# Performance work log

Hardware: AMD Instinct MI355X
Metric: run time of the kernel (lower is better)

## Reference

```python
import jax, jax.numpy as jnp
import numpy as np

# dims: B graphs, NE entity nodes, NR relation nodes, N total nodes, D=hsz, H heads, P prop steps
B, NE, NR, D, H, P = 4, 1536, 512, 128, 4, 2
N = NE + NR
DH = D // H
RV = 500  # relation vocab
EPS = 1e-5


def setup_inputs() -> dict:
    key = jax.random.key(0)
    ks = jax.random.split(key, 20)
    s = 0.02
    inp = {
        "vents": jax.random.normal(ks[0], (B, NE, D), dtype=jnp.float32),
        "rels": jax.random.randint(ks[1], (B, NR), 0, RV),
        "adj": jax.random.randint(ks[2], (B, N, N), 0, 2, dtype=jnp.int32),
        "entlens": jnp.full((B,), NE, dtype=jnp.int32),
        "renc_w": jax.random.normal(ks[3], (RV, D), dtype=jnp.float32) * s,
        # per-prop-step attention params (torch Linear stored as [in, out])
        "Wq": jax.random.normal(ks[4], (P, D, D)) * s,
        "bq": jnp.zeros((P, D)),
        "Wk": jax.random.normal(ks[5], (P, D, D)) * s,
        "bk": jnp.zeros((P, D)),
        "Wv": jax.random.normal(ks[6], (P, D, D)) * s,
        "bv": jnp.zeros((P, D)),
        "Wo": jax.random.normal(ks[7], (P, D, D)) * s,
        "bo": jnp.zeros((P, D)),
        # Block FFN hsz -> 4*hsz -> hsz
        "l1_w": jax.random.normal(ks[8], (P, D, 4 * D)) * s,
        "l1_b": jnp.zeros((P, 4 * D)),
        "l2_w": jax.random.normal(ks[9], (P, 4 * D, D)) * s,
        "l2_b": jnp.zeros((P, D)),
        # ln_1 is used for BOTH norms in Block (faithful to original bug)
        "ln_g": jnp.ones((P, D)),
        "ln_b": jnp.zeros((P, D)),
        # PReLU per-channel slope, torch default 0.25
        "prelu_a": jnp.full((P, 4 * D), 0.25, dtype=jnp.float32),
    }
    return inp


def _ln(x, g, b):
    m = x.mean(-1, keepdims=True)
    v = ((x - m) ** 2).mean(-1, keepdims=True)
    return (x - m) / jnp.sqrt(v + EPS) * g + b


def reference(vents, rels, adj, entlens, renc_w,
              Wq, bq, Wk, bk, Wv, bv, Wo, bo,
              l1_w, l1_b, l2_w, l2_b, ln_g, ln_b, prelu_a):
    # vgraph_i = cat(vents[i][:entlens[i]], renc(rels[i])) -> all graphs same size, batched
    vgraph = jnp.concatenate([vents, renc_w[rels]], axis=1)  # [B, N, D]
    mask = (adj == 0)  # [B, N, N] True = masked out
    scale = 1.0 / np.sqrt(DH).astype(np.float32)
    for p in range(P):
        q_in = vgraph
        kv_in = jax.lax.stop_gradient(vgraph)  # dense path: ngraph is detached
        Q = (q_in @ Wq[p] + bq[p]).reshape(B, N, H, DH)
        K = (kv_in @ Wk[p] + bk[p]).reshape(B, N, H, DH)
        V = (kv_in @ Wv[p] + bv[p]).reshape(B, N, H, DH)
        scores = jnp.einsum('bihd,bjhd->bhij', Q, K) * scale  # [B, H, N, N]
        scores = jnp.where(mask[:, None, :, :], -1e9, scores)
        A = jax.nn.softmax(scores, axis=-1)
        O = jnp.einsum('bhij,bjhd->bihd', A, V).reshape(B, N, D) @ Wo[p] + bo[p]
        # Block feed-forward (dropout = identity in eval)
        t = _ln(O, ln_g[p], ln_b[p])
        h1 = t @ l1_w[p] + l1_b[p]
        h1 = jnp.where(h1 >= 0, h1, prelu_a[p] * h1)  # PReLU
        q2 = h1 @ l2_w[p] + l2_b[p]
        vgraph = _ln(q2 + t, ln_g[p], ln_b[p])
    glob = vgraph[jnp.arange(B), entlens]  # vgraph[entlens[i]] per graph -> [B, D]
    gents = vgraph  # all graphs same length, no padding needed -> [B, N, D]
    emask = jnp.ones((B, N), dtype=bool)  # arange(N) <= N is all True
    return glob, gents, emask
```

## Files before the change

kernel.cpp:

```cpp
#include <hip/hip_runtime.h>
#include <hip/hip_bf16.h>

typedef __bf16 bf16;
typedef __bf16 bf16x4 __attribute__((ext_vector_type(4)));
typedef __bf16 bf16x8 __attribute__((ext_vector_type(8)));
typedef float f32x4 __attribute__((ext_vector_type(4)));
typedef float f32x16 __attribute__((ext_vector_type(16)));

#define B_ 4
#define NE_ 1536
#define NR_ 512
#define N_ 2048
#define D_ 128
#define H_ 4
#define DH_ 32
#define P_ 2
#define M_ (B_*N_)
#define NW_ (N_/32)
#define SK_ 4
#define KCH_ (N_/SK_)
#define NIT_ (KCH_/64)

__device__ __forceinline__ f32x4 mfma16(bf16x8 a, bf16x8 b, f32x4 c) {
    return __builtin_amdgcn_mfma_f32_16x16x32_bf16(a, b, c, 0, 0, 0);
}
__device__ __forceinline__ f32x16 mfma32(bf16x8 a, bf16x8 b, f32x16 c) {
    return __builtin_amdgcn_mfma_f32_32x32x16_bf16(a, b, c, 0, 0, 0);
}
__device__ __forceinline__ unsigned cvtpk(float lo, float hi) {
    unsigned r;
    asm("v_cvt_pk_bf16_f32 %0, %1, %2" : "=v"(r) : "v"(lo), "v"(hi));
    return r;
}
__device__ __forceinline__ void swap32(unsigned& a, unsigned& b) {
    asm("v_permlane32_swap_b32 %0, %1" : "+v"(a), "+v"(b));
}
__device__ __forceinline__ void gload16(const void* g, void* l) {
    __builtin_amdgcn_global_load_lds(
        (const __attribute__((address_space(1))) void*)g,
        (__attribute__((address_space(3))) void*)l, 16, 0, 0);
}

__device__ __forceinline__ size_t fragidx(int c, int i, int K) {
    int nb = c >> 4, kc = i >> 5;
    int l = ((i >> 3) & 3) * 16 + (c & 15);
    return ((size_t)(nb * (K >> 5) + kc) * 64 + l) * 8 + (i & 7);
}

#define VGN_ (B_*N_*D_)
#define MKN_ (B_*N_*NW_)
#define PPER_ (3*16384 + 16384 + 65536 + 65536 + 384)
#define PRN_ (P_*PPER_)
__global__ void k_prep(const float* __restrict__ vents, const int* __restrict__ rels,
                       const float* __restrict__ renc, const int* __restrict__ adj,
                       const float* __restrict__ Wq, const float* __restrict__ Wk,
                       const float* __restrict__ Wv, const float* __restrict__ Wo,
                       const float* __restrict__ l1w, const float* __restrict__ l2w,
                       const float* __restrict__ bq, const float* __restrict__ bk,
                       const float* __restrict__ bv,
                       bf16* __restrict__ vb, unsigned int* __restrict__ mw,
                       bf16* __restrict__ wqkvT, float* __restrict__ bqkv,
                       bf16* __restrict__ woT, bf16* __restrict__ l1T,
                       bf16* __restrict__ l2T) {
    const float SC = 0.25503330560513437f;
    int idx = blockIdx.x * 256 + threadIdx.x;
    if (idx < VGN_) {
        int d = idx & (D_ - 1);
        int n = (idx >> 7) & (N_ - 1);
        int b = idx >> 18;
        float v;
        if (n < NE_) v = vents[((size_t)(b * NE_ + n)) * D_ + d];
        else         v = renc[(size_t)rels[b * NR_ + (n - NE_)] * D_ + d];
        vb[idx] = (bf16)v;
        return;
    }
    idx -= VGN_;
    if (idx < MKN_) {
        const int4* a = (const int4*)(adj + (size_t)idx * 32);
        unsigned int w = 0;
#pragma unroll
        for (int q = 0; q < 8; ++q) {
            int4 t = a[q];
            w |= (t.x != 0 ? 1u : 0u) << (q * 4 + 0);
            w |= (t.y != 0 ? 1u : 0u) << (q * 4 + 1);
            w |= (t.z != 0 ? 1u : 0u) << (q * 4 + 2);
            w |= (t.w != 0 ? 1u : 0u) << (q * 4 + 3);
        }
        mw[idx] = w;
        return;
    }
    idx -= MKN_;
    if (idx >= PRN_) return;
    int p = idx / PPER_;
    int r = idx % PPER_;
    if (r < 3 * 16384) {
        int which = r / 16384, e = r % 16384;
        int o = e >> 7, i = e & 127;
        const float* W = which == 0 ? Wq : (which == 1 ? Wk : Wv);
        float v = W[(size_t)(p * 128 + i) * 128 + o];
        if (which == 0) v *= SC;
        wqkvT[(size_t)p * 384 * 128 + fragidx(which * 128 + o, i, 128)] = (bf16)v;
    } else if ((r -= 3 * 16384) < 16384) {
        int o = r >> 7, i = r & 127;
        woT[(size_t)p * 16384 + fragidx(o, i, 128)] = (bf16)Wo[(size_t)(p * 128 + i) * 128 + o];
    } else if ((r -= 16384) < 65536) {
        int o = r >> 7, i = r & 127;
        l1T[(size_t)p * 65536 + fragidx(o, i, 128)] = (bf16)l1w[(size_t)(p * 128 + i) * 512 + o];
    } else if ((r -= 65536) < 65536) {
        int o = r >> 9, i = r & 511;
        l2T[(size_t)p * 65536 + fragidx(o, i, 512)] = (bf16)l2w[(size_t)(p * 512 + i) * 128 + o];
    } else {
        r -= 65536;
        float v = r < 128 ? bq[p * 128 + r] * SC
                          : (r < 256 ? bk[p * 128 + r - 128] : bv[p * 128 + r - 256]);
        bqkv[p * 384 + r] = v;
    }
}

__global__ __launch_bounds__(256) void k_qkv(
        const bf16* __restrict__ X, const bf16* __restrict__ WT,
        const float* __restrict__ bias,
        bf16* __restrict__ Qout, bf16* __restrict__ Kout,
        bf16* __restrict__ VTout) {
    int lane = threadIdx.x & 63, wid = threadIdx.x >> 6;
    int wr = wid >> 1, wc = wid & 1;
    int m0 = blockIdx.x * 64 + wr * 32;
    int n0 = blockIdx.y * 64 + wc * 32;
    int lr = lane & 15, lg = lane >> 4;
    f32x4 acc[2][2];
#pragma unroll
    for (int mi = 0; mi < 2; ++mi)
#pragma unroll
        for (int ni = 0; ni < 2; ++ni)
            acc[mi][ni] = f32x4{0.f, 0.f, 0.f, 0.f};

    for (int k0 = 0; k0 < 128; k0 += 32) {
        int kc = k0 >> 5;
        bf16x8 a[2], bb[2];
#pragma unroll
        for (int mi = 0; mi < 2; ++mi)
            a[mi] = *(const bf16x8*)(X + (size_t)(m0 + mi * 16 + lr) * 128 + k0 + lg * 8);
#pragma unroll
        for (int ni = 0; ni < 2; ++ni) {
            int nb = (n0 >> 4) + ni;
            bb[ni] = *(const bf16x8*)(WT + ((size_t)(nb * 4 + kc) * 64 + lane) * 8);
        }
#pragma unroll
        for (int mi = 0; mi < 2; ++mi)
#pragma unroll
            for (int ni = 0; ni < 2; ++ni)
                acc[mi][ni] = mfma16(a[mi], bb[ni], acc[mi][ni]);
    }
#pragma unroll
    for (int mi = 0; mi < 2; ++mi) {
#pragma unroll
        for (int ni = 0; ni < 2; ++ni) {
            int col = n0 + ni * 16 + lr;
            float bs = bias[col];
            int rowb = m0 + mi * 16 + lg * 4;
            if (col < 128) {
#pragma unroll
                for (int r = 0; r < 4; ++r)
                    Qout[(size_t)(rowb + r) * D_ + col] = (bf16)(acc[mi][ni][r] + bs);
            } else if (col < 256) {
#pragma unroll
                for (int r = 0; r < 4; ++r)
                    Kout[(size_t)(rowb + r) * D_ + (col - 128)] = (bf16)(acc[mi][ni][r] + bs);
            } else {
                int d = col - 256, h = d >> 5, dh = d & 31;
                int b = rowb >> 11, nn = rowb & (N_ - 1);
                bf16x4 pk;
#pragma unroll
                for (int r = 0; r < 4; ++r) pk[r] = (bf16)(acc[mi][ni][r] + bs);
                *(bf16x4*)(VTout + ((size_t)(b * H_ + h) * DH_ + dh) * N_ + nn) = pk;
            }
        }
    }
}

__global__ __launch_bounds__(256) void k_attn(
    const bf16* __restrict__ Q, const bf16* __restrict__ Kt,
    const bf16* __restrict__ VT, const unsigned int* __restrict__ mw,
    bf16* __restrict__ partO, float* __restrict__ partML) {
    __shared__ __align__(16) char kbuf[3][4096];
    __shared__ __align__(16) char vbuf[3][4096];
    __shared__ __align__(16) unsigned mbuf[128][16];
    int wid = threadIdx.x >> 6;
    int lane = threadIdx.x & 63;
    int ql = lane & 31, hf = lane >> 5;
    int qx = blockIdx.x;
    int bh = blockIdx.y;
    int kc = blockIdx.z;
    int b = bh >> 2, h = bh & 3;
    int qg = qx * 128 + wid * 32 + ql;
    const size_t bnD = (size_t)b * N_ * D_;

    const bf16* qp = Q + bnD + (size_t)qg * D_ + h * 32 + hf * 8;
    bf16x8 qf0 = *(const bf16x8*)(qp);
    bf16x8 qf1 = *(const bf16x8*)(qp + 16);

#pragma unroll
    for (int j = 0; j < 2; ++j) {
        int u = threadIdx.x + 256 * j;
        int row = u >> 2, sub = u & 3;
        uint4 mv = *(const uint4*)(mw + ((size_t)b * N_ + qx * 128 + row) * NW_
                                      + kc * (KCH_ / 32) + sub * 4);
        *(uint4*)(&mbuf[row][sub * 4]) = mv;
    }
    asm volatile("s_waitcnt lgkmcnt(0)" ::: "memory");

    const char* kg = (const char*)(Kt + bnD + (size_t)(kc * KCH_) * D_) + h * 64;
    const char* vg = (const char*)(VT + (size_t)(bh * DH_) * N_ + kc * KCH_);

    f32x16 of;
#pragma unroll
    for (int i = 0; i < 16; ++i) of[i] = 0.f;
    const f32x16 zero16 = of;
    float lsum = 0.f;
    int mrow = wid * 32 + ql;

#define STAGE(bufi, it) do {                                                   \
        int k0s = (it) * 64;                                                   \
        gload16(kg + (size_t)(k0s + lane) * 256 + wid * 16,                    \
                kbuf[bufi] + wid * 1024);                                      \
        gload16(vg + ((size_t)(lane & 31) * N_ + k0s) * 2 +                    \
                    (2 * wid + (lane >> 5)) * 16,                              \
                vbuf[bufi] + wid * 1024);                                      \
    } while (0)

    STAGE(0, 0);
    STAGE(1, 1);
    __builtin_amdgcn_s_barrier();

    unsigned long long mcur = *(const unsigned long long*)(&mbuf[mrow][0]);

#pragma unroll 1
    for (int it = 0; it < NIT_; ++it) {
        int cur = it % 3;
        const char* kb_ = kbuf[cur];
        const char* vb_ = vbuf[cur];
        if (it < NIT_ - 1) asm volatile("s_waitcnt vmcnt(2)" ::: "memory");
        else               asm volatile("s_waitcnt vmcnt(0)" ::: "memory");
        __builtin_amdgcn_s_barrier();
        __builtin_amdgcn_sched_barrier(0);
        if (it + 2 < NIT_) STAGE((it + 2) % 3, it + 2);

        unsigned long long mnext = (it + 1 < NIT_)
            ? *(const unsigned long long*)(&mbuf[mrow][(it + 1) * 2]) : 0ull;
        unsigned mw0 = (unsigned)mcur, mw1 = (unsigned)(mcur >> 32);

#pragma unroll
        for (int kb = 0; kb < 2; ++kb) {
            bf16x8 kf0 = *(const bf16x8*)(kb_ + hf * 1024 + (kb * 32 + ql) * 16);
            bf16x8 kf1 = *(const bf16x8*)(kb_ + 2048 + hf * 1024 + (kb * 32 + ql) * 16);
            f32x16 s = mfma32(kf0, qf0, zero16);
            s = mfma32(kf1, qf1, s);

            unsigned wsh = (kb ? mw1 : mw0) >> (hf * 4);
            float p[16];
#pragma unroll
            for (int r = 0; r < 16; ++r) {
                int bitp = (r & 3) + 8 * (r >> 2);
                float e = __builtin_amdgcn_exp2f(s[r]);
                p[r] = ((wsh >> bitp) & 1u) ? e : 0.f;
            }
            float a0 = (p[0] + p[1]) + (p[2] + p[3]);
            float a1 = (p[4] + p[5]) + (p[6] + p[7]);
            float a2 = (p[8] + p[9]) + (p[10] + p[11]);
            float a3 = (p[12] + p[13]) + (p[14] + p[15]);
            lsum += (a0 + a1) + (a2 + a3);

            unsigned lo0 = cvtpk(p[0], p[1]),   hi0 = cvtpk(p[2], p[3]);
            unsigned lo1 = cvtpk(p[4], p[5]),   hi1 = cvtpk(p[6], p[7]);
            unsigned lo2 = cvtpk(p[8], p[9]),   hi2 = cvtpk(p[10], p[11]);
            unsigned lo3 = cvtpk(p[12], p[13]), hi3 = cvtpk(p[14], p[15]);
            swap32(lo0, lo1); swap32(hi0, hi1);
            swap32(lo2, lo3); swap32(hi2, hi3);
            union { unsigned u[4]; bf16x8 v; } f0, f1;
            f0.u[0] = lo0; f0.u[1] = hi0; f0.u[2] = lo1; f0.u[3] = hi1;
            f1.u[0] = lo2; f1.u[1] = hi2; f1.u[2] = lo3; f1.u[3] = hi3;

            bf16x8 va = *(const bf16x8*)(vb_ + ((kb * 2 + 0) * 2 + hf) * 512 + ql * 16);
            bf16x8 vb2 = *(const bf16x8*)(vb_ + ((kb * 2 + 1) * 2 + hf) * 512 + ql * 16);
            __builtin_amdgcn_s_setprio(1);
            of = mfma32(va, f0.v, of);
            of = mfma32(vb2, f1.v, of);
            __builtin_amdgcn_s_setprio(0);
        }
        mcur = mnext;
    }
#undef STAGE

    lsum += __shfl_xor(lsum, 32, 64);
    size_t pb = ((size_t)(kc * 16 + bh) * N_ + qg) * 32;
#pragma unroll
    for (int g = 0; g < 4; ++g) {
        union { unsigned u[2]; bf16x4 v; } pk;
        pk.u[0] = cvtpk(of[4 * g + 0], of[4 * g + 1]);
        pk.u[1] = cvtpk(of[4 * g + 2], of[4 * g + 3]);
        *(bf16x4*)(partO + pb + 8 * g + 4 * hf) = pk.v;
    }
    if (lane < 32)
        partML[(size_t)(kc * 16 + bh) * N_ + qg] = lsum;
}

template <bool LAST>
__global__ __launch_bounds__(512) void k_ffn(
        const bf16* __restrict__ partO, const float* __restrict__ partML,
        const bf16* __restrict__ woT, const float* __restrict__ bo,
        const bf16* __restrict__ l1T, const float* __restrict__ l1b,
        const float* __restrict__ pra,
        const bf16* __restrict__ l2T, const float* __restrict__ l2b,
        const float* __restrict__ lng, const float* __restrict__ lnb,
        const bf16* __restrict__ wqkvT2, const float* __restrict__ bqkv2,
        const int* __restrict__ entl, float* __restrict__ gout,
        bf16* __restrict__ Qout, bf16* __restrict__ Kout,
        bf16* __restrict__ VTout) {
    __shared__ __align__(16) char Obuf[16 * 256];
    __shared__ __align__(16) char Tbuf[16 * 256];
    __shared__ __align__(16) char Hbuf[16 * 1024];
    __shared__ float lst[8][16][2];
    int t = threadIdx.x;
    int lane = t & 63, wid = t >> 6;
    int lr = lane & 15, lg = lane >> 4;
    int m0 = blockIdx.x * 16;

    {
        int i = t >> 5, u = t & 31;
        int r = m0 + i, b = r >> 11, q = r & (N_ - 1);
        int h = u >> 3, dh4 = u & 7;
        int bh = b * 4 + h;
        float L = 0.f;
        f32x4 o = {0.f, 0.f, 0.f, 0.f};
#pragma unroll
        for (int kc = 0; kc < SK_; ++kc) {
            size_t base = (size_t)(kc * 16 + bh) * N_ + q;
            L += partML[base];
            bf16x4 pv = *(const bf16x4*)(partO + base * 32 + dh4 * 4);
#pragma unroll
            for (int j = 0; j < 4; ++j) o[j] += (float)pv[j];
        }
        float rL = 1.f / L;
        bf16x4 pk;
#pragma unroll
        for (int j = 0; j < 4; ++j) pk[j] = (bf16)(o[j] * rL);
        *(bf16x4*)(Obuf + i * 256 + ((u * 8) ^ ((i & 7) << 4))) = pk;
    }
    __syncthreads();

    float tvx[4];
    {
        f32x4 acc = {0.f, 0.f, 0.f, 0.f};
#pragma unroll
        for (int k0 = 0; k0 < 128; k0 += 32) {
            bf16x8 a = *(const bf16x8*)(Obuf + lr * 256 + (((k0 + lg * 8) * 2) ^ ((lr & 7) << 4)));
            bf16x8 bb = *(const bf16x8*)(woT + ((size_t)(wid * 4 + (k0 >> 5)) * 64 + lane) * 8);
            acc = mfma16(a, bb, acc);
        }
        int col = wid * 16 + lr;
        float bs = bo[col];
#pragma unroll
        for (int r2 = 0; r2 < 4; ++r2) tvx[r2] = acc[r2] + bs;
#pragma unroll
        for (int r2 = 0; r2 < 4; ++r2) {
            float sv = tvx[r2], qv = tvx[r2] * tvx[r2];
#pragma unroll
            for (int msk = 1; msk < 16; msk <<= 1) {
                sv += __shfl_xor(sv, msk, 64);
                qv += __shfl_xor(qv, msk, 64);
            }
            if (lr == 0) { lst[wid][lg * 4 + r2][0] = sv; lst[wid][lg * 4 + r2][1] = qv; }
        }
        __syncthreads();
#pragma unroll
        for (int r2 = 0; r2 < 4; ++r2) {
            int row = lg * 4 + r2;
            float S = 0.f, Q2 = 0.f;
#pragma unroll
            for (int w2 = 0; w2 < 8; ++w2) { S += lst[w2][row][0]; Q2 += lst[w2][row][1]; }
            float mean = S * (1.f / 128.f);
            float var = Q2 * (1.f / 128.f) - mean * mean;
            float rstd = rsqrtf(var + 1e-5f);
            float o = (tvx[r2] - mean) * rstd * lng[col] + lnb[col];
            tvx[r2] = o;
            *(bf16*)(Tbuf + row * 256 + ((col * 2) ^ ((row & 7) << 4))) = (bf16)o;
        }
    }
    __syncthreads();

    {
        f32x4 acc[4];
#pragma unroll
        for (int ni = 0; ni < 4; ++ni) acc[ni] = f32x4{0.f, 0.f, 0.f, 0.f};
#pragma unroll
        for (int k0 = 0; k0 < 128; k0 += 32) {
            bf16x8 a = *(const bf16x8*)(Tbuf + lr * 256 + (((k0 + lg * 8) * 2) ^ ((lr & 7) << 4)));
#pragma unroll
            for (int ni = 0; ni < 4; ++ni) {
                bf16x8 bb = *(const bf16x8*)(l1T + ((size_t)((wid * 4 + ni) * 4 + (k0 >> 5)) * 64 + lane) * 8);
                acc[ni] = mfma16(a, bb, acc[ni]);
            }
        }
#pragma unroll
        for (int ni = 0; ni < 4; ++ni) {
            int col = wid * 64 + ni * 16 + lr;
            float bs = l1b[col], sl = pra[col];
#pragma unroll
            for (int r2 = 0; r2 < 4; ++r2) {
                int row = lg * 4 + r2;
                float v = acc[ni][r2] + bs;
                v = v >= 0.f ? v : sl * v;
                *(bf16*)(Hbuf + row * 1024 + ((col * 2) ^ ((row & 7) << 4))) = (bf16)v;
            }
        }
    }
    __syncthreads();

    {
        f32x4 acc = {0.f, 0.f, 0.f, 0.f};
#pragma unroll
        for (int k0 = 0; k0 < 512; k0 += 32) {
            bf16x8 a = *(const bf16x8*)(Hbuf + lr * 1024 + (((k0 + lg * 8) * 2) ^ ((lr & 7) << 4)));
            bf16x8 bb = *(const bf16x8*)(l2T + ((size_t)(wid * 16 + (k0 >> 5)) * 64 + lane) * 8);
            acc = mfma16(a, bb, acc);
        }
        int col = wid * 16 + lr;
        float bs = l2b[col];
        float vx[4];
#pragma unroll
        for (int r2 = 0; r2 < 4; ++r2)
            vx[r2] = acc[r2] + bs + tvx[r2];
        __syncthreads();
#pragma unroll
        for (int r2 = 0; r2 < 4; ++r2) {
            float sv = vx[r2], qv = vx[r2] * vx[r2];
#pragma unroll
            for (int msk = 1; msk < 16; msk <<= 1) {
                sv += __shfl_xor(sv, msk, 64);
                qv += __shfl_xor(qv, msk, 64);
            }
            if (lr == 0) { lst[wid][lg * 4 + r2][0] = sv; lst[wid][lg * 4 + r2][1] = qv; }
        }
        __syncthreads();
#pragma unroll
        for (int r2 = 0; r2 < 4; ++r2) {
            int row = lg * 4 + r2;
            float S = 0.f, Q2 = 0.f;
#pragma unroll
            for (int w2 = 0; w2 < 8; ++w2) { S += lst[w2][row][0]; Q2 += lst[w2][row][1]; }
            float mean = S * (1.f / 128.f);
            float var = Q2 * (1.f / 128.f) - mean * mean;
            float rstd = rsqrtf(var + 1e-5f);
            float o = (vx[r2] - mean) * rstd * lng[col] + lnb[col];
            size_t rowg = (size_t)(m0 + row);
            if (LAST) {
                float* gents = gout + 512;
                gents[rowg * 128 + col] = o;
                int b = (int)(rowg >> 11);
                if ((int)(rowg & (N_ - 1)) == entl[b])
                    gout[b * 128 + col] = o;
            } else {
                *(bf16*)(Obuf + row * 256 + ((col * 2) ^ ((row & 7) << 4))) = (bf16)o;
            }
        }
        if (LAST && t < 16)
            gout[512 + (size_t)M_ * 128 + m0 + t] = 1.0f;
    }

    if (!LAST) {
        __syncthreads();
        f32x4 acc[3];
#pragma unroll
        for (int ni = 0; ni < 3; ++ni) acc[ni] = f32x4{0.f, 0.f, 0.f, 0.f};
#pragma unroll
        for (int k0 = 0; k0 < 128; k0 += 32) {
            bf16x8 a = *(const bf16x8*)(Obuf + lr * 256 + (((k0 + lg * 8) * 2) ^ ((lr & 7) << 4)));
#pragma unroll
            for (int ni = 0; ni < 3; ++ni) {
                bf16x8 bb = *(const bf16x8*)(wqkvT2 + ((size_t)((wid * 3 + ni) * 4 + (k0 >> 5)) * 64 + lane) * 8);
                acc[ni] = mfma16(a, bb, acc[ni]);
            }
        }
#pragma unroll
        for (int ni = 0; ni < 3; ++ni) {
            int col = wid * 48 + ni * 16 + lr;
            float bs = bqkv2[col];
            int rowb = m0 + lg * 4;
            if (col < 128) {
#pragma unroll
                for (int r = 0; r < 4; ++r)
                    Qout[(size_t)(rowb + r) * D_ + col] = (bf16)(acc[ni][r] + bs);
            } else if (col < 256) {
#pragma unroll
                for (int r = 0; r < 4; ++r)
                    Kout[(size_t)(rowb + r) * D_ + (col - 128)] = (bf16)(acc[ni][r] + bs);
            } else {
                int d = col - 256, h = d >> 5, dh = d & 31;
                int b = rowb >> 11, nn = rowb & (N_ - 1);
                bf16x4 pk;
#pragma unroll
                for (int r = 0; r < 4; ++r) pk[r] = (bf16)(acc[ni][r] + bs);
                *(bf16x4*)(VTout + ((size_t)(b * H_ + h) * DH_ + dh) * N_ + nn) = pk;
            }
        }
    }
}

extern "C" void kernel_launch(void* const* d_in, const int* in_sizes, int n_in,
                              void* d_out, int out_size, void* d_ws, size_t ws_size,
                              hipStream_t stream) {
    const float* vents = (const float*)d_in[0];
    const int*   rels  = (const int*)d_in[1];
    const int*   adj   = (const int*)d_in[2];
    const int*   entl  = (const int*)d_in[3];
    const float* renc  = (const float*)d_in[4];
    const float* Wq = (const float*)d_in[5];
    const float* bq = (const float*)d_in[6];
    const float* Wk = (const float*)d_in[7];
    const float* bk = (const float*)d_in[8];
    const float* Wv = (const float*)d_in[9];
    const float* bv = (const float*)d_in[10];
    const float* Wo = (const float*)d_in[11];
    const float* bo = (const float*)d_in[12];
    const float* l1w = (const float*)d_in[13];
    const float* l1b = (const float*)d_in[14];
    const float* l2w = (const float*)d_in[15];
    const float* l2b = (const float*)d_in[16];
    const float* lng = (const float*)d_in[17];
    const float* lnb = (const float*)d_in[18];
    const float* pra = (const float*)d_in[19];

    char* w = (char*)d_ws;
    auto alloc = [&](size_t bytes) { char* r = w; w += (bytes + 255) & ~(size_t)255; return r; };
    bf16*  vb    = (bf16*)alloc((size_t)M_ * D_ * 2);
    unsigned int* mw = (unsigned int*)alloc((size_t)B_ * N_ * NW_ * 4);
    bf16*  wqkvT = (bf16*)alloc((size_t)P_ * 384 * 128 * 2);
    float* bqkv  = (float*)alloc((size_t)P_ * 384 * 4);
    bf16*  woT   = (bf16*)alloc((size_t)P_ * 128 * 128 * 2);
    bf16*  l1T   = (bf16*)alloc((size_t)P_ * 512 * 128 * 2);
    bf16*  l2T   = (bf16*)alloc((size_t)P_ * 128 * 512 * 2);
    bf16*  Qb    = (bf16*)alloc((size_t)M_ * D_ * 2);
    bf16*  Kb    = (bf16*)alloc((size_t)M_ * D_ * 2);
    bf16*  VTb   = (bf16*)alloc((size_t)M_ * D_ * 2);
    bf16*  partO  = (bf16*)alloc((size_t)SK_ * 16 * N_ * 32 * 2);
    float* partML = (float*)alloc((size_t)SK_ * 16 * N_ * 4);
    float* gout  = (float*)d_out;

    const int PRTOT = VGN_ + MKN_ + PRN_;
    k_prep<<<(PRTOT + 255) / 256, 256, 0, stream>>>(
        vents, rels, renc, adj, Wq, Wk, Wv, Wo, l1w, l2w, bq, bk, bv,
        vb, mw, wqkvT, bqkv, woT, l1T, l2T);
    k_qkv<<<dim3(M_ / 64, 384 / 64), 256, 0, stream>>>(
        vb, wqkvT, bqkv, Qb, Kb, VTb);
    k_attn<<<dim3(16, 16, SK_), 256, 0, stream>>>(Qb, Kb, VTb, mw, partO, partML);
    k_ffn<false><<<M_ / 16, 512, 0, stream>>>(
        partO, partML, woT, bo, l1T, l1b, pra, l2T, l2b, lng, lnb,
        wqkvT + (size_t)384 * 128, bqkv + 384, entl, nullptr, Qb, Kb, VTb);
    k_attn<<<dim3(16, 16, SK_), 256, 0, stream>>>(Qb, Kb, VTb, mw, partO, partML);
    k_ffn<true><<<M_ / 16, 512, 0, stream>>>(
        partO, partML, woT + (size_t)16384, bo + 128,
        l1T + (size_t)65536, l1b + 512, pra + 512,
        l2T + (size_t)65536, l2b + 128, lng + 128, lnb + 128,
        wqkvT, bqkv, entl, gout, Qb, Kb, VTb);
}
```

Measured before the change: 108.3 us.

## Fuse first-step QKV projection into prep kernel and pad attention mask LDS

Removes the separate k_qkv launch and the bf16 vgraph staging buffer. The first propagation step's QKV GEMM now runs inside k_prep: it gathers fp32 rows straight from vents or the relation embedding table and converts weights on the fly, in the same launch as the mask packing and weight transposition. This saves one kernel launch and a full activation round trip through memory. In exchange, the weight loads are strided, uncoalesced scalar fp32 reads repeated by every block. Separately, the attention mask LDS rows are padded from 16 to 18 words, with stores split into 8-byte halves, to reduce bank conflicts.

```diff
diff --git a/kernel.cpp b/kernel.cpp
--- a/kernel.cpp
+++ b/kernel.cpp
@@ -47,34 +47,105 @@
     return ((size_t)(nb * (K >> 5) + kc) * 64 + l) * 8 + (i & 7);
 }
 
-#define VGN_ (B_*N_*D_)
+#define QKVB_ 768
 #define MKN_ (B_*N_*NW_)
 #define PPER_ (3*16384 + 16384 + 65536 + 65536 + 384)
 #define PRN_ (P_*PPER_)
-__global__ void k_prep(const float* __restrict__ vents, const int* __restrict__ rels,
-                       const float* __restrict__ renc, const int* __restrict__ adj,
-                       const float* __restrict__ Wq, const float* __restrict__ Wk,
-                       const float* __restrict__ Wv, const float* __restrict__ Wo,
-                       const float* __restrict__ l1w, const float* __restrict__ l2w,
-                       const float* __restrict__ bq, const float* __restrict__ bk,
-                       const float* __restrict__ bv,
-                       bf16* __restrict__ vb, unsigned int* __restrict__ mw,
-                       bf16* __restrict__ wqkvT, float* __restrict__ bqkv,
-                       bf16* __restrict__ woT, bf16* __restrict__ l1T,
-                       bf16* __restrict__ l2T) {
+__global__ __launch_bounds__(256) void k_prep(
+        const float* __restrict__ vents, const int* __restrict__ rels,
+        const float* __restrict__ renc, const int* __restrict__ adj,
+        const float* __restrict__ Wq, const float* __restrict__ Wk,
+        const float* __restrict__ Wv, const float* __restrict__ Wo,
+        const float* __restrict__ l1w, const float* __restrict__ l2w,
+        const float* __restrict__ bq, const float* __restrict__ bk,
+        const float* __restrict__ bv,
+        unsigned int* __restrict__ mw,
+        bf16* __restrict__ wqkvT, float* __restrict__ bqkv,
+        bf16* __restrict__ woT, bf16* __restrict__ l1T,
+        bf16* __restrict__ l2T,
+        bf16* __restrict__ Qout, bf16* __restrict__ Kout,
+        bf16* __restrict__ VTout) {
     const float SC = 0.25503330560513437f;
-    int idx = blockIdx.x * 256 + threadIdx.x;
-    if (idx < VGN_) {
-        int d = idx & (D_ - 1);
-        int n = (idx >> 7) & (N_ - 1);
-        int b = idx >> 18;
-        float v;
-        if (n < NE_) v = vents[((size_t)(b * NE_ + n)) * D_ + d];
-        else         v = renc[(size_t)rels[b * NR_ + (n - NE_)] * D_ + d];
-        vb[idx] = (bf16)v;
+    if (blockIdx.x < QKVB_) {
+        int qb = blockIdx.x;
+        int mt = qb / 6, nt = qb % 6;
+        int lane = threadIdx.x & 63, wid = threadIdx.x >> 6;
+        int wr = wid >> 1, wc = wid & 1;
+        int m0 = mt * 64 + wr * 32;
+        int n0 = nt * 64 + wc * 32;
+        int lr = lane & 15, lg = lane >> 4;
+        const float* srcA[2];
+#pragma unroll
+        for (int mi = 0; mi < 2; ++mi) {
+            int row = m0 + mi * 16 + lr;
+            int n = row & (N_ - 1), b = row >> 11;
+            srcA[mi] = (n < NE_) ? vents + ((size_t)(b * NE_ + n)) * D_
+                                 : renc + (size_t)rels[b * NR_ + (n - NE_)] * D_;
+        }
+        f32x4 acc[2][2];
+#pragma unroll
+        for (int mi = 0; mi < 2; ++mi)
+#pragma unroll
+            for (int ni = 0; ni < 2; ++ni)
+                acc[mi][ni] = f32x4{0.f, 0.f, 0.f, 0.f};
+        for (int k0 = 0; k0 < 128; k0 += 32) {
+            bf16x8 a[2], bb[2];
+#pragma unroll
+            for (int mi = 0; mi < 2; ++mi) {
+                float4 f0 = *(const float4*)(srcA[mi] + k0 + lg * 8);
+                float4 f1 = *(const float4*)(srcA[mi] + k0 + lg * 8 + 4);
+                bf16x8 v;
+                v[0] = (bf16)f0.x; v[1] = (bf16)f0.y; v[2] = (bf16)f0.z; v[3] = (bf16)f0.w;
+                v[4] = (bf16)f1.x; v[5] = (bf16)f1.y; v[6] = (bf16)f1.z; v[7] = (bf16)f1.w;
+                a[mi] = v;
+            }
+#pragma unroll
+            for (int ni = 0; ni < 2; ++ni) {
+                int col = n0 + ni * 16 + lr;
+                int which = col >> 7, c0 = col & 127;
+                const float* W = which == 0 ? Wq : (which == 1 ? Wk : Wv);
+                float sc = which == 0 ? SC : 1.f;
+                bf16x8 v;
+#pragma unroll
+                for (int e = 0; e < 8; ++e)
+                    v[e] = (bf16)(W[(size_t)(k0 + lg * 8 + e) * 128 + c0] * sc);
+                bb[ni] = v;
+            }
+#pragma unroll
+            for (int mi = 0; mi < 2; ++mi)
+#pragma unroll
+                for (int ni = 0; ni < 2; ++ni)
+                    acc[mi][ni] = mfma16(a[mi], bb[ni], acc[mi][ni]);
+        }
+#pragma unroll
+        for (int mi = 0; mi < 2; ++mi) {
+#pragma unroll
+            for (int ni = 0; ni < 2; ++ni) {
+                int col = n0 + ni * 16 + lr;
+                int which = col >> 7, c0 = col & 127;
+                float bs = which == 0 ? bq[c0] * SC : (which == 1 ? bk[c0] : bv[c0]);
+                int rowb = m0 + mi * 16 + lg * 4;
+                if (which == 0) {
+#pragma unroll
+                    for (int r = 0; r < 4; ++r)
+                        Qout[(size_t)(rowb + r) * D_ + c0] = (bf16)(acc[mi][ni][r] + bs);
+                } else if (which == 1) {
+#pragma unroll
+                    for (int r = 0; r < 4; ++r)
+                        Kout[(size_t)(rowb + r) * D_ + c0] = (bf16)(acc[mi][ni][r] + bs);
+                } else {
+                    int h = c0 >> 5, dh = c0 & 31;
+                    int b = rowb >> 11, nn = rowb & (N_ - 1);
+                    bf16x4 pk;
+#pragma unroll
+                    for (int r = 0; r < 4; ++r) pk[r] = (bf16)(acc[mi][ni][r] + bs);
+                    *(bf16x4*)(VTout + ((size_t)(b * H_ + h) * DH_ + dh) * N_ + nn) = pk;
+                }
+            }
+        }
         return;
     }
-    idx -= VGN_;
+    int idx = (blockIdx.x - QKVB_) * 256 + threadIdx.x;
     if (idx < MKN_) {
         const int4* a = (const int4*)(adj + (size_t)idx * 32);
         unsigned int w = 0;
@@ -117,74 +188,13 @@
     }
 }
 
-__global__ __launch_bounds__(256) void k_qkv(
-        const bf16* __restrict__ X, const bf16* __restrict__ WT,
-        const float* __restrict__ bias,
-        bf16* __restrict__ Qout, bf16* __restrict__ Kout,
-        bf16* __restrict__ VTout) {
-    int lane = threadIdx.x & 63, wid = threadIdx.x >> 6;
-    int wr = wid >> 1, wc = wid & 1;
-    int m0 = blockIdx.x * 64 + wr * 32;
-    int n0 = blockIdx.y * 64 + wc * 32;
-    int lr = lane & 15, lg = lane >> 4;
-    f32x4 acc[2][2];
-#pragma unroll
-    for (int mi = 0; mi < 2; ++mi)
-#pragma unroll
-        for (int ni = 0; ni < 2; ++ni)
-            acc[mi][ni] = f32x4{0.f, 0.f, 0.f, 0.f};
-
-    for (int k0 = 0; k0 < 128; k0 += 32) {
-        int kc = k0 >> 5;
-        bf16x8 a[2], bb[2];
-#pragma unroll
-        for (int mi = 0; mi < 2; ++mi)
-            a[mi] = *(const bf16x8*)(X + (size_t)(m0 + mi * 16 + lr) * 128 + k0 + lg * 8);
-#pragma unroll
-        for (int ni = 0; ni < 2; ++ni) {
-            int nb = (n0 >> 4) + ni;
-            bb[ni] = *(const bf16x8*)(WT + ((size_t)(nb * 4 + kc) * 64 + lane) * 8);
-        }
-#pragma unroll
-        for (int mi = 0; mi < 2; ++mi)
-#pragma unroll
-            for (int ni = 0; ni < 2; ++ni)
-                acc[mi][ni] = mfma16(a[mi], bb[ni], acc[mi][ni]);
-    }
-#pragma unroll
-    for (int mi = 0; mi < 2; ++mi) {
-#pragma unroll
-        for (int ni = 0; ni < 2; ++ni) {
-            int col = n0 + ni * 16 + lr;
-            float bs = bias[col];
-            int rowb = m0 + mi * 16 + lg * 4;
-            if (col < 128) {
-#pragma unroll
-                for (int r = 0; r < 4; ++r)
-                    Qout[(size_t)(rowb + r) * D_ + col] = (bf16)(acc[mi][ni][r] + bs);
-            } else if (col < 256) {
-#pragma unroll
-                for (int r = 0; r < 4; ++r)
-                    Kout[(size_t)(rowb + r) * D_ + (col - 128)] = (bf16)(acc[mi][ni][r] + bs);
-            } else {
-                int d = col - 256, h = d >> 5, dh = d & 31;
-                int b = rowb >> 11, nn = rowb & (N_ - 1);
-                bf16x4 pk;
-#pragma unroll
-                for (int r = 0; r < 4; ++r) pk[r] = (bf16)(acc[mi][ni][r] + bs);
-                *(bf16x4*)(VTout + ((size_t)(b * H_ + h) * DH_ + dh) * N_ + nn) = pk;
-            }
-        }
-    }
-}
-
 __global__ __launch_bounds__(256) void k_attn(
     const bf16* __restrict__ Q, const bf16* __restrict__ Kt,
     const bf16* __restrict__ VT, const unsigned int* __restrict__ mw,
     bf16* __restrict__ partO, float* __restrict__ partML) {
     __shared__ __align__(16) char kbuf[3][4096];
     __shared__ __align__(16) char vbuf[3][4096];
-    __shared__ __align__(16) unsigned mbuf[128][16];
+    __shared__ __align__(16) unsigned mbuf[128][18];
     int wid = threadIdx.x >> 6;
     int lane = threadIdx.x & 63;
     int ql = lane & 31, hf = lane >> 5;
@@ -205,7 +215,10 @@
         int row = u >> 2, sub = u & 3;
         uint4 mv = *(const uint4*)(mw + ((size_t)b * N_ + qx * 128 + row) * NW_
                                       + kc * (KCH_ / 32) + sub * 4);
-        *(uint4*)(&mbuf[row][sub * 4]) = mv;
+        uint2 lo; lo.x = mv.x; lo.y = mv.y;
+        uint2 hi; hi.x = mv.z; hi.y = mv.w;
+        *(uint2*)(&mbuf[row][sub * 4]) = lo;
+        *(uint2*)(&mbuf[row][sub * 4 + 2]) = hi;
     }
     asm volatile("s_waitcnt lgkmcnt(0)" ::: "memory");
 
@@ -532,7 +545,6 @@
 
     char* w = (char*)d_ws;
     auto alloc = [&](size_t bytes) { char* r = w; w += (bytes + 255) & ~(size_t)255; return r; };
-    bf16*  vb    = (bf16*)alloc((size_t)M_ * D_ * 2);
     unsigned int* mw = (unsigned int*)alloc((size_t)B_ * N_ * NW_ * 4);
     bf16*  wqkvT = (bf16*)alloc((size_t)P_ * 384 * 128 * 2);
     float* bqkv  = (float*)alloc((size_t)P_ * 384 * 4);
@@ -546,12 +558,10 @@
     float* partML = (float*)alloc((size_t)SK_ * 16 * N_ * 4);
     float* gout  = (float*)d_out;
 
-    const int PRTOT = VGN_ + MKN_ + PRN_;
-    k_prep<<<(PRTOT + 255) / 256, 256, 0, stream>>>(
+    const int PRB = QKVB_ + (MKN_ + PRN_ + 255) / 256;
+    k_prep<<<PRB, 256, 0, stream>>>(
         vents, rels, renc, adj, Wq, Wk, Wv, Wo, l1w, l2w, bq, bk, bv,
-        vb, mw, wqkvT, bqkv, woT, l1T, l2T);
-    k_qkv<<<dim3(M_ / 64, 384 / 64), 256, 0, stream>>>(
-        vb, wqkvT, bqkv, Qb, Kb, VTb);
+        mw, wqkvT, bqkv, woT, l1T, l2T, Qb, Kb, VTb);
     k_attn<<<dim3(16, 16, SK_), 256, 0, stream>>>(Qb, Kb, VTb, mw, partO, partML);
     k_ffn<false><<<M_ / 16, 512, 0, stream>>>(
         partO, partML, woT, bo, l1T, l1b, pra, l2T, l2b, lng, lnb,
```

After: 106.8 us, median of 2. Within noise of the previous version (-1.4%).
